# Kernel tuning notes

Hardware: AMD Instinct MI355X
Metric: run time of the kernel (lower is better)

Reference implementation:

```python
import jax, jax.numpy as jnp
import numpy as np

B, T, D, N, R, K = 4, 4096, 1024, 64, 16, 4  # batch, seq, d_model, state_size, dt_rank, conv_kernel


def setup_inputs() -> dict:
    key = jax.random.key(0)
    ks = jax.random.split(key, 6)
    s = 0.02  # small init scale (original uses xavier/zeros; random here for a meaningful baseline)
    return {
        "x": jax.random.normal(ks[0], (B, T, D), jnp.float32),
        "conv_w": jax.random.normal(ks[1], (D, K), jnp.float32) * s,  # depthwise conv kernel [D, K]
        "in_w": jax.random.normal(ks[2], (N, D), jnp.float32) * s,    # input_proj weight
        "in_b": jnp.zeros((N,), jnp.float32),
        "dt_w": jax.random.normal(ks[3], (R, D), jnp.float32) * s,    # delta_proj weight
        "dt_b": jnp.zeros((R,), jnp.float32),
        "tr_w": jax.random.normal(ks[4], (N, R), jnp.float32) * s,    # transition weight (no bias)
        "out_w": jax.random.normal(ks[5], (D, N), jnp.float32) * s,   # output_proj weight
        "out_b": jnp.zeros((D,), jnp.float32),
    }


def reference(x, conv_w, in_w, in_b, dt_w, dt_b, tr_w, out_w, out_b):
    Bx, Tx, Dx = x.shape
    k = conv_w.shape[1]
    # Causal depthwise conv: torch Conv1d(pad=k-1, groups=D) then slice [:T]
    xp = jnp.pad(x, ((0, 0), (k - 1, 0), (0, 0)))  # left-pad time axis
    conv_out = sum(xp[:, j:j + Tx, :] * conv_w[:, j] for j in range(k))  # [B,T,D]
    projected = (x + conv_out) @ in_w.T + in_b                 # [B,T,N]
    delta = jnp.tanh(x @ dt_w.T + dt_b) @ tr_w.T               # [B,T,N]

    def step(state, inp):
        d_t, p_t = inp  # each [B,N]
        state = jax.nn.silu(d_t + state) + p_t
        return state, state

    init = jnp.zeros((Bx, in_w.shape[0]), x.dtype)
    _, states = jax.lax.scan(step, init,
                             (jnp.swapaxes(delta, 0, 1), jnp.swapaxes(projected, 0, 1)))
    states = jnp.swapaxes(states, 0, 1)  # [B,T,N]
    return states @ out_w.T + out_b      # [B,T,D] (dropout=0.0 -> identity)
```

## Files before the change

kernel.cpp:

```cpp
#include <hip/hip_runtime.h>
#include <math.h>

#define Bn 4
#define Tn 4096
#define Dn 1024
#define Nn 64
#define Rn 16
#define KCONV 4

#define TT2 32
#define KCH 32
#define SU 32

typedef __attribute__((ext_vector_type(8))) short bf16x8;
typedef __attribute__((ext_vector_type(4))) float f32x4;

__device__ __forceinline__ unsigned short bf16_rne(float f) {
    unsigned int u = __float_as_uint(f);
    unsigned int r = (u + 0x7fffu + ((u >> 16) & 1u)) >> 16;
    return (unsigned short)r;
}

typedef const __attribute__((address_space(1))) void GVoid;
typedef __attribute__((address_space(3))) void LVoid;
typedef __attribute__((address_space(3))) float LdsFloat;


__global__ __launch_bounds__(256)
void prep0_kernel(const float* __restrict__ in_w, const float* __restrict__ dt_w,
                  unsigned short* __restrict__ ws)
{
    const int kc  = blockIdx.x;
    const int k0  = kc * KCH;
    const int tid = threadIdx.x;
    unsigned short* wsb = ws + (size_t)kc * 5120;

    {
        const int lane = tid & 63;
        const int n = (tid >> 6) * 16 + (lane & 15), s = lane >> 4;
        const float* wp = &in_w[(size_t)n * Dn + k0 + 8 * s];
        float4 a  = *(const float4*)wp;
        float4 bq = *(const float4*)(wp + 4);
        float wv[8] = {a.x, a.y, a.z, a.w, bq.x, bq.y, bq.z, bq.w};
        bf16x8 fh, fl;
        #pragma unroll
        for (int k = 0; k < 8; ++k) {
            unsigned short h = bf16_rne(wv[k]);
            float hf = __uint_as_float((unsigned)h << 16);
            fh[k] = (short)h; fl[k] = (short)bf16_rne(wv[k] - hf);
        }
        *(bf16x8*)&wsb[(size_t)tid * 8]        = fh;
        *(bf16x8*)&wsb[2048 + (size_t)tid * 8] = fl;
    }
    if (tid < 64) {
        const int r = tid & 15, s = tid >> 4;
        const float* wp = &dt_w[(size_t)r * Dn + k0 + 8 * s];
        float4 a  = *(const float4*)wp;
        float4 bq = *(const float4*)(wp + 4);
        float wv[8] = {a.x, a.y, a.z, a.w, bq.x, bq.y, bq.z, bq.w};
        bf16x8 fh, fl;
        #pragma unroll
        for (int k = 0; k < 8; ++k) {
            unsigned short h = bf16_rne(wv[k]);
            float hf = __uint_as_float((unsigned)h << 16);
            fh[k] = (short)h; fl[k] = (short)bf16_rne(wv[k] - hf);
        }
        *(bf16x8*)&wsb[4096 + (size_t)tid * 8] = fh;
        *(bf16x8*)&wsb[4608 + (size_t)tid * 8] = fl;
    }
}

__global__ __launch_bounds__(128)
void prep_kernel(const float* __restrict__ x, const float* __restrict__ conv_w,
                 const unsigned short* __restrict__ ws,
                 const float* __restrict__ in_b, const float* __restrict__ dt_b,
                 const float* __restrict__ tr_w,
                 float* __restrict__ O)
{
    __shared__ bf16x8 Axc_h[2][64], Axc_l[2][64];
    __shared__ bf16x8 Axr_h[2][64], Axr_l[2][64];
    __shared__ bf16x8 Bst[640];
    __shared__ float  xs[35][36];
    __shared__ float4 cws[32];
    __shared__ float  AsS[TT2][17];
    __shared__ float  trS[Nn][17];

    const int tid = threadIdx.x;
    const int b   = blockIdx.y;
    const int t0  = blockIdx.x * TT2;
    const int l   = tid & 63;
    const int w   = tid >> 6;

    const float* xb = x + (size_t)b * Tn * Dn;

    for (int idx = tid; idx < Nn * Rn; idx += 128)
        trS[idx >> 4][idx & 15] = tr_w[idx];

    const f32x4 z4 = {0.f, 0.f, 0.f, 0.f};
    f32x4 accP[4] = {z4, z4, z4, z4};
    f32x4 accG = z4;

    for (int kc = 0; kc < Dn / KCH; ++kc) {
        const int k0 = kc * KCH;
        __syncthreads();

        if (tid < 64) {
            const unsigned short* wsb = ws + (size_t)kc * 5120 + (size_t)l * 8;
            #pragma unroll
            for (int j = 0; j < 10; ++j)
                __builtin_amdgcn_global_load_lds((GVoid*)(wsb + j * 512),
                                                 (LVoid*)(Bst + j * 64), 16, 0, 0);
        }

        {
            const int row  = tid >> 2;
            const int colg = tid & 3;
            const int tp   = t0 - 3 + row;
            float4 a = {0.f,0.f,0.f,0.f}, bq = {0.f,0.f,0.f,0.f};
            if (tp >= 0) {
                const float* src = &xb[(size_t)tp * Dn + k0 + 8 * colg];
                a  = *(const float4*)src;
                bq = *(const float4*)(src + 4);
            }
            *(float4*)&xs[row][8 * colg]     = a;
            *(float4*)&xs[row][8 * colg + 4] = bq;
            if (tid < 12) {
                const int row2 = 32 + (tid >> 2), colg2 = tid & 3;
                const float* s2 = &xb[(size_t)(t0 - 3 + row2) * Dn + k0 + 8 * colg2];
                *(float4*)&xs[row2][8 * colg2]     = *(const float4*)s2;
                *(float4*)&xs[row2][8 * colg2 + 4] = *(const float4*)(s2 + 4);
            }
            if (tid >= 64 && tid < 96)
                cws[tid - 64] = *(const float4*)&conv_w[(size_t)(k0 + tid - 64) * 4];
        }
        __syncthreads();

        {
            const int m = tid & 31;
            const int s = tid >> 5;
            float v[4][8];
            #pragma unroll
            for (int dr = 0; dr < 4; ++dr) {
                float4 a  = *(const float4*)&xs[m + dr][8 * s];
                float4 bq = *(const float4*)&xs[m + dr][8 * s + 4];
                v[dr][0]=a.x;  v[dr][1]=a.y;  v[dr][2]=a.z;  v[dr][3]=a.w;
                v[dr][4]=bq.x; v[dr][5]=bq.y; v[dr][6]=bq.z; v[dr][7]=bq.w;
            }
            bf16x8 fch, fcl, frh, frl;
            #pragma unroll
            for (int k = 0; k < 8; ++k) {
                float4 cw = cws[8 * s + k];
                float xr = v[3][k];
                float xc = xr;
                xc = fmaf(v[0][k], cw.x, xc);
                xc = fmaf(v[1][k], cw.y, xc);
                xc = fmaf(v[2][k], cw.z, xc);
                xc = fmaf(v[3][k], cw.w, xc);
                unsigned short h; float hf;
                h = bf16_rne(xc); hf = __uint_as_float((unsigned)h << 16);
                fch[k] = (short)h; fcl[k] = (short)bf16_rne(xc - hf);
                h = bf16_rne(xr); hf = __uint_as_float((unsigned)h << 16);
                frh[k] = (short)h; frl[k] = (short)bf16_rne(xr - hf);
            }
            const int lane = (m & 15) | (s << 4), mt = m >> 4;
            Axc_h[mt][lane] = fch; Axc_l[mt][lane] = fcl;
            Axr_h[mt][lane] = frh; Axr_l[mt][lane] = frl;
        }
        __syncthreads();

        bf16x8 axh = Axc_h[w][l], axl = Axc_l[w][l];
        bf16x8 arh = Axr_h[w][l], arl = Axr_l[w][l];
        #pragma unroll
        for (int nt = 0; nt < 4; ++nt) {
            bf16x8 bh = Bst[nt * 64 + l];
            bf16x8 bl = Bst[256 + nt * 64 + l];
            accP[nt] = __builtin_amdgcn_mfma_f32_16x16x32_bf16(axh, bh, accP[nt], 0, 0, 0);
            accP[nt] = __builtin_amdgcn_mfma_f32_16x16x32_bf16(axl, bh, accP[nt], 0, 0, 0);
            accP[nt] = __builtin_amdgcn_mfma_f32_16x16x32_bf16(axh, bl, accP[nt], 0, 0, 0);
        }
        {
            bf16x8 bh = Bst[512 + l];
            bf16x8 bl = Bst[576 + l];
            accG = __builtin_amdgcn_mfma_f32_16x16x32_bf16(arh, bh, accG, 0, 0, 0);
            accG = __builtin_amdgcn_mfma_f32_16x16x32_bf16(arl, bh, accG, 0, 0, 0);
            accG = __builtin_amdgcn_mfma_f32_16x16x32_bf16(arh, bl, accG, 0, 0, 0);
        }
    }

    __syncthreads();
    #pragma unroll
    for (int i = 0; i < 4; ++i)
        AsS[16 * w + 4 * (l >> 4) + i][l & 15] = tanhf(accG[i] + dt_b[l & 15]);
    __syncthreads();

    float as_[4][16];
    #pragma unroll
    for (int i = 0; i < 4; ++i) {
        int mrow = 16 * w + 4 * (l >> 4) + i;
        #pragma unroll
        for (int j = 0; j < 4; ++j) {
            float4 q = *(const float4*)&AsS[mrow][4 * j];
            as_[i][4*j] = q.x; as_[i][4*j+1] = q.y;
            as_[i][4*j+2] = q.z; as_[i][4*j+3] = q.w;
        }
    }
    const int tile0 = t0 & ~63;
    const int coff  = t0 & 63;
    #pragma unroll
    for (int nt = 0; nt < 4; ++nt) {
        int n = 16 * nt + (l & 15);
        float tw[16];
        #pragma unroll
        for (int j = 0; j < 4; ++j) {
            float4 q = *(const float4*)&trS[n][4 * j];
            tw[4*j] = q.x; tw[4*j+1] = q.y; tw[4*j+2] = q.z; tw[4*j+3] = q.w;
        }
        float ib = in_b[n];
        #pragma unroll
        for (int i = 0; i < 4; ++i) {
            int mrow = 16 * w + 4 * (l >> 4) + i;
            float dlv = 0.f;
            #pragma unroll
            for (int r = 0; r < 16; ++r) dlv = fmaf(as_[i][r], tw[r], dlv);
            size_t a = ((size_t)(b * Tn + tile0 + n)) * Dn + coff + mrow;
            O[a]      = accP[nt][i] + ib;
            O[a + 64] = dlv;
        }
    }
}


#define WAITV(N) do {                                                    \
    asm volatile("s_waitcnt vmcnt(" #N ")" ::: "memory");                \
    __builtin_amdgcn_sched_barrier(0);                                   \
} while (0)

__device__ __forceinline__ void issue_chunk(float* lds, const float* rp)
{
    #pragma unroll
    for (int j = 0; j < 8; ++j)
        __builtin_amdgcn_global_load_lds((GVoid*)(rp + 4 * j),
                                         (LVoid*)(lds + j * 256), 16, 0, 0);
    #pragma unroll
    for (int j = 0; j < 8; ++j)
        __builtin_amdgcn_global_load_lds((GVoid*)(rp + 64 + 4 * j),
                                         (LVoid*)(lds + (8 + j) * 256), 16, 0, 0);
}

#define DS_READ_ALL(pv, dv, a)                                           \
    asm volatile(                                                        \
        "ds_read_b128 %0, %16 offset:0\n\t"                              \
        "ds_read_b128 %1, %16 offset:1024\n\t"                           \
        "ds_read_b128 %2, %16 offset:2048\n\t"                           \
        "ds_read_b128 %3, %16 offset:3072\n\t"                           \
        "ds_read_b128 %4, %16 offset:4096\n\t"                           \
        "ds_read_b128 %5, %16 offset:5120\n\t"                           \
        "ds_read_b128 %6, %16 offset:6144\n\t"                           \
        "ds_read_b128 %7, %16 offset:7168\n\t"                           \
        "ds_read_b128 %8, %16 offset:8192\n\t"                           \
        "ds_read_b128 %9, %16 offset:9216\n\t"                           \
        "ds_read_b128 %10, %16 offset:10240\n\t"                         \
        "ds_read_b128 %11, %16 offset:11264\n\t"                         \
        "ds_read_b128 %12, %16 offset:12288\n\t"                         \
        "ds_read_b128 %13, %16 offset:13312\n\t"                         \
        "ds_read_b128 %14, %16 offset:14336\n\t"                         \
        "ds_read_b128 %15, %16 offset:15360\n\t"                         \
        "s_waitcnt lgkmcnt(0)"                                           \
        : "=&v"(pv[0]), "=&v"(pv[1]), "=&v"(pv[2]), "=&v"(pv[3]),        \
          "=&v"(pv[4]), "=&v"(pv[5]), "=&v"(pv[6]), "=&v"(pv[7]),        \
          "=&v"(dv[0]), "=&v"(dv[1]), "=&v"(dv[2]), "=&v"(dv[3]),        \
          "=&v"(dv[4]), "=&v"(dv[5]), "=&v"(dv[6]), "=&v"(dv[7])         \
        : "v"(a) : "memory")

__device__ __forceinline__ void scan_chunk(const float* buf, int n, float& st,
                                           f32x4 (&sv)[8], float* sp)
{
    const float L2E = 1.44269504088896340736f;
    if (sp) {
        #pragma unroll
        for (int j = 0; j < 8; ++j)
            *(f32x4*)(sp + 4 * j) = sv[j];
    }
    unsigned a = (unsigned)(unsigned long long)(LdsFloat*)buf
               + (unsigned)(n * 16);
    f32x4 pv[8], dv[8];
    DS_READ_ALL(pv, dv, a);
    __builtin_amdgcn_sched_barrier(0);
    #pragma unroll
    for (int j = 0; j < 8; ++j) {
        #pragma unroll
        for (int i = 0; i < 4; ++i) {
            float d  = dv[j][i];
            float u  = st + d;
            float e  = __builtin_amdgcn_exp2f(fmaf(st, -L2E, -d * L2E));
            float r  = __builtin_amdgcn_rcpf(1.f + e);
            st = fmaf(u, r, pv[j][i]);
            sv[j][i] = st;
        }
    }
}

#define RP(c) (obase + (size_t)((((c) >> 1) * 64) + n) * Dn + ((c) & 1) * 32)
#define SP(c) (RP(c) + 128)

__global__ __launch_bounds__(64, 1)
void scan_kernel(float* __restrict__ O)
{
    __shared__ __align__(16) float buf[3][4096];

    const int b = blockIdx.x;
    const int n = threadIdx.x;
    float* obase = O + (size_t)b * Tn * Dn;

    float* b0 = buf[0];
    float* b1 = buf[1];
    float* b2 = buf[2];

    f32x4 sv[8];
    float st = 0.f;

    issue_chunk(b0, RP(0));
    issue_chunk(b1, RP(1));
    issue_chunk(b2, RP(2));
    WAITV(32);
    scan_chunk(b0, n, st, sv, nullptr);
    { float* t = b0; b0 = b1; b1 = b2; b2 = t; }

    issue_chunk(b2, RP(3));
    WAITV(32);
    scan_chunk(b0, n, st, sv, SP(0));
    { float* t = b0; b0 = b1; b1 = b2; b2 = t; }

    #pragma unroll 1
    for (int c = 2; c <= 125; ++c) {
        issue_chunk(b2, RP(c + 2));
        WAITV(40);
        scan_chunk(b0, n, st, sv, SP(c - 1));
        { float* t = b0; b0 = b1; b1 = b2; b2 = t; }
    }

    WAITV(24);
    scan_chunk(b0, n, st, sv, SP(125));
    { float* t = b0; b0 = b1; b1 = b2; b2 = t; }

    WAITV(16);
    scan_chunk(b0, n, st, sv, SP(126));

    {
        float* sp = SP(127);
        #pragma unroll
        for (int j = 0; j < 8; ++j)
            *(f32x4*)(sp + 4 * j) = sv[j];
    }
}

#undef RP
#undef SP

__global__ __launch_bounds__(256)
void out_kernel(const float* __restrict__ out_w, const float* __restrict__ out_b,
                float* __restrict__ O)
{
    __shared__ float Ss[64][Nn + 4];
    __shared__ float wT[Nn][64 + 4];

    const int tid = threadIdx.x;
    const int r0  = blockIdx.x * 64;
    const int c   = tid & 15;
    const int g   = tid >> 4;

    float4 wreg[4];
    #pragma unroll
    for (int q = 0; q < 4; ++q) {
        int idx = tid + q * 256;
        int dl = idx >> 4, n4 = (idx & 15) * 4;
        wreg[q] = *(const float4*)&out_w[(size_t)dl * Nn + n4];
    }

    for (int idx = tid; idx < 64 * 16; idx += 256) {
        int nn = idx >> 4, tg = idx & 15;
        float4 v = *(const float4*)&O[(size_t)(r0 + nn) * Dn + 128 + 4 * tg];
        Ss[4 * tg + 0][nn] = v.x;
        Ss[4 * tg + 1][nn] = v.y;
        Ss[4 * tg + 2][nn] = v.z;
        Ss[4 * tg + 3][nn] = v.w;
    }
    __syncthreads();

    for (int cb = 0; cb < Dn / 64; ++cb) {
        #pragma unroll
        for (int q = 0; q < 4; ++q) {
            int idx = tid + q * 256;
            int dl = idx >> 4, n4 = (idx & 15) * 4;
            wT[n4 + 0][dl] = wreg[q].x;
            wT[n4 + 1][dl] = wreg[q].y;
            wT[n4 + 2][dl] = wreg[q].z;
            wT[n4 + 3][dl] = wreg[q].w;
        }
        if (cb + 1 < Dn / 64) {
            const int d0n = (cb + 1) * 64;
            #pragma unroll
            for (int q = 0; q < 4; ++q) {
                int idx = tid + q * 256;
                int dl = idx >> 4, n4 = (idx & 15) * 4;
                wreg[q] = *(const float4*)&out_w[(size_t)(d0n + dl) * Nn + n4];
            }
        }
        __syncthreads();

        const int d0 = cb * 64;
        float acc[4][4] = {};
        #pragma unroll
        for (int kq = 0; kq < Nn; kq += 4) {
            float4 wv0 = *(const float4*)&wT[kq + 0][4 * c];
            float4 wv1 = *(const float4*)&wT[kq + 1][4 * c];
            float4 wv2 = *(const float4*)&wT[kq + 2][4 * c];
            float4 wv3 = *(const float4*)&wT[kq + 3][4 * c];
            #pragma unroll
            for (int i = 0; i < 4; ++i) {
                int row = g + 16 * i;
                float4 xv = *(const float4*)&Ss[row][kq];
                acc[i][0] = fmaf(xv.x, wv0.x, fmaf(xv.y, wv1.x, fmaf(xv.z, wv2.x, fmaf(xv.w, wv3.x, acc[i][0]))));
                acc[i][1] = fmaf(xv.x, wv0.y, fmaf(xv.y, wv1.y, fmaf(xv.z, wv2.y, fmaf(xv.w, wv3.y, acc[i][1]))));
                acc[i][2] = fmaf(xv.x, wv0.z, fmaf(xv.y, wv1.z, fmaf(xv.z, wv2.z, fmaf(xv.w, wv3.z, acc[i][2]))));
                acc[i][3] = fmaf(xv.x, wv0.w, fmaf(xv.y, wv1.w, fmaf(xv.z, wv2.w, fmaf(xv.w, wv3.w, acc[i][3]))));
            }
        }

        float4 bb = *(const float4*)&out_b[d0 + 4 * c];
        #pragma unroll
        for (int i = 0; i < 4; ++i) {
            int row = g + 16 * i;
            float4 o = make_float4(acc[i][0] + bb.x, acc[i][1] + bb.y,
                                   acc[i][2] + bb.z, acc[i][3] + bb.w);
            *(float4*)&O[(size_t)(r0 + row) * Dn + d0 + 4 * c] = o;
        }
        __syncthreads();
    }
}

extern "C" void kernel_launch(void* const* d_in, const int* in_sizes, int n_in,
                              void* d_out, int out_size, void* d_ws, size_t ws_size,
                              hipStream_t stream)
{
    const float* x      = (const float*)d_in[0];
    const float* conv_w = (const float*)d_in[1];
    const float* in_w   = (const float*)d_in[2];
    const float* in_b   = (const float*)d_in[3];
    const float* dt_w   = (const float*)d_in[4];
    const float* dt_b   = (const float*)d_in[5];
    const float* tr_w   = (const float*)d_in[6];
    const float* out_w  = (const float*)d_in[7];
    const float* out_b  = (const float*)d_in[8];
    float* O = (float*)d_out;
    unsigned short* ws = (unsigned short*)d_ws;
    (void)ws_size;

    prep0_kernel<<<dim3(Dn / KCH), 256, 0, stream>>>(in_w, dt_w, ws);

    dim3 g1(Tn / TT2, Bn);
    prep_kernel<<<g1, 128, 0, stream>>>(x, conv_w, ws, in_b, dt_b, tr_w, O);

    scan_kernel<<<dim3(Bn), 64, 0, stream>>>(O);

    out_kernel<<<dim3((Bn * Tn) / 64), 256, 0, stream>>>(out_w, out_b, O);
}
```

Before: 337.4 us.

## Move output projection to bf16x3 split MFMA with pre-split weights

The fp32 FMA output projection is replaced by MFMA 16x16x32 bf16 instructions that use a hi/lo split (three products) to keep near-fp32 accuracy. out_w is pre-split into bf16 hi/lo fragments in the prep kernel and streamed into LDS with async global-to-LDS loads, double-buffered per wave. The goal is to cut the out_kernel's ALU-bound time. In exchange the outputs are written as scattered scalar stores, and the bf16x3 scheme carries a small risk of precision loss.

```diff
diff --git a/kernel.cpp b/kernel.cpp
--- a/kernel.cpp
+++ b/kernel.cpp
@@ -28,45 +28,68 @@
 
 __global__ __launch_bounds__(256)
 void prep0_kernel(const float* __restrict__ in_w, const float* __restrict__ dt_w,
-                  unsigned short* __restrict__ ws)
-{
-    const int kc  = blockIdx.x;
-    const int k0  = kc * KCH;
+                  const float* __restrict__ out_w, unsigned short* __restrict__ ws)
+{
     const int tid = threadIdx.x;
-    unsigned short* wsb = ws + (size_t)kc * 5120;
-
-    {
-        const int lane = tid & 63;
-        const int n = (tid >> 6) * 16 + (lane & 15), s = lane >> 4;
-        const float* wp = &in_w[(size_t)n * Dn + k0 + 8 * s];
-        float4 a  = *(const float4*)wp;
-        float4 bq = *(const float4*)(wp + 4);
-        float wv[8] = {a.x, a.y, a.z, a.w, bq.x, bq.y, bq.z, bq.w};
-        bf16x8 fh, fl;
-        #pragma unroll
-        for (int k = 0; k < 8; ++k) {
-            unsigned short h = bf16_rne(wv[k]);
-            float hf = __uint_as_float((unsigned)h << 16);
-            fh[k] = (short)h; fl[k] = (short)bf16_rne(wv[k] - hf);
-        }
-        *(bf16x8*)&wsb[(size_t)tid * 8]        = fh;
-        *(bf16x8*)&wsb[2048 + (size_t)tid * 8] = fl;
-    }
-    if (tid < 64) {
-        const int r = tid & 15, s = tid >> 4;
-        const float* wp = &dt_w[(size_t)r * Dn + k0 + 8 * s];
-        float4 a  = *(const float4*)wp;
-        float4 bq = *(const float4*)(wp + 4);
-        float wv[8] = {a.x, a.y, a.z, a.w, bq.x, bq.y, bq.z, bq.w};
-        bf16x8 fh, fl;
-        #pragma unroll
-        for (int k = 0; k < 8; ++k) {
-            unsigned short h = bf16_rne(wv[k]);
-            float hf = __uint_as_float((unsigned)h << 16);
-            fh[k] = (short)h; fl[k] = (short)bf16_rne(wv[k] - hf);
-        }
-        *(bf16x8*)&wsb[4096 + (size_t)tid * 8] = fh;
-        *(bf16x8*)&wsb[4608 + (size_t)tid * 8] = fl;
+    if (blockIdx.x < 32) {
+        const int kc  = blockIdx.x;
+        const int k0  = kc * KCH;
+        unsigned short* wsb = ws + (size_t)kc * 5120;
+        {
+            const int lane = tid & 63;
+            const int n = (tid >> 6) * 16 + (lane & 15), s = lane >> 4;
+            const float* wp = &in_w[(size_t)n * Dn + k0 + 8 * s];
+            float4 a  = *(const float4*)wp;
+            float4 bq = *(const float4*)(wp + 4);
+            float wv[8] = {a.x, a.y, a.z, a.w, bq.x, bq.y, bq.z, bq.w};
+            bf16x8 fh, fl;
+            #pragma unroll
+            for (int k = 0; k < 8; ++k) {
+                unsigned short h = bf16_rne(wv[k]);
+                float hf = __uint_as_float((unsigned)h << 16);
+                fh[k] = (short)h; fl[k] = (short)bf16_rne(wv[k] - hf);
+            }
+            *(bf16x8*)&wsb[(size_t)tid * 8]        = fh;
+            *(bf16x8*)&wsb[2048 + (size_t)tid * 8] = fl;
+        }
+        if (tid < 64) {
+            const int r = tid & 15, s = tid >> 4;
+            const float* wp = &dt_w[(size_t)r * Dn + k0 + 8 * s];
+            float4 a  = *(const float4*)wp;
+            float4 bq = *(const float4*)(wp + 4);
+            float wv[8] = {a.x, a.y, a.z, a.w, bq.x, bq.y, bq.z, bq.w};
+            bf16x8 fh, fl;
+            #pragma unroll
+            for (int k = 0; k < 8; ++k) {
+                unsigned short h = bf16_rne(wv[k]);
+                float hf = __uint_as_float((unsigned)h << 16);
+                fh[k] = (short)h; fl[k] = (short)bf16_rne(wv[k] - hf);
+            }
+            *(bf16x8*)&wsb[4096 + (size_t)tid * 8] = fh;
+            *(bf16x8*)&wsb[4608 + (size_t)tid * 8] = fl;
+        }
+    } else {
+        const int dt = blockIdx.x - 32;
+        if (tid < 128) {
+            const int kh = tid >> 6, lane = tid & 63;
+            const int d  = dt * 16 + (lane & 15);
+            const int n0 = kh * 32 + (lane >> 4) * 8;
+            const float* wp = &out_w[(size_t)d * Nn + n0];
+            float4 a  = *(const float4*)wp;
+            float4 bq = *(const float4*)(wp + 4);
+            float wv[8] = {a.x, a.y, a.z, a.w, bq.x, bq.y, bq.z, bq.w};
+            bf16x8 fh, fl;
+            #pragma unroll
+            for (int k = 0; k < 8; ++k) {
+                unsigned short h = bf16_rne(wv[k]);
+                float hf = __uint_as_float((unsigned)h << 16);
+                fh[k] = (short)h; fl[k] = (short)bf16_rne(wv[k] - hf);
+            }
+            unsigned short* wsb = ws + 163840 + (size_t)dt * 2048
+                                + (size_t)kh * 1024 + (size_t)lane * 8;
+            *(bf16x8*)wsb         = fh;
+            *(bf16x8*)(wsb + 512) = fl;
+        }
     }
 }
 
@@ -357,25 +380,35 @@
 #undef RP
 #undef SP
 
+
+#define DS_READ_B8(b00h, b00l, b01h, b01l, b10h, b10l, b11h, b11l, a)    \
+    asm volatile(                                                        \
+        "ds_read_b128 %0, %8 offset:0\n\t"                               \
+        "ds_read_b128 %1, %8 offset:1024\n\t"                            \
+        "ds_read_b128 %2, %8 offset:2048\n\t"                            \
+        "ds_read_b128 %3, %8 offset:3072\n\t"                            \
+        "ds_read_b128 %4, %8 offset:4096\n\t"                            \
+        "ds_read_b128 %5, %8 offset:5120\n\t"                            \
+        "ds_read_b128 %6, %8 offset:6144\n\t"                            \
+        "ds_read_b128 %7, %8 offset:7168\n\t"                            \
+        "s_waitcnt lgkmcnt(0)"                                           \
+        : "=&v"(b00h), "=&v"(b00l), "=&v"(b01h), "=&v"(b01l),            \
+          "=&v"(b10h), "=&v"(b10l), "=&v"(b11h), "=&v"(b11l)             \
+        : "v"(a) : "memory")
+
 __global__ __launch_bounds__(256)
-void out_kernel(const float* __restrict__ out_w, const float* __restrict__ out_b,
-                float* __restrict__ O)
-{
-    __shared__ float Ss[64][Nn + 4];
-    __shared__ float wT[Nn][64 + 4];
+void out_kernel(const unsigned short* __restrict__ ws,
+                const float* __restrict__ out_b, float* __restrict__ O)
+{
+    __shared__ float  Ss[64][Nn + 4];
+    __shared__ bf16x8 AfH[8][64], AfL[8][64];
+    __shared__ bf16x8 Bb[4][2][8][64];
 
     const int tid = threadIdx.x;
     const int r0  = blockIdx.x * 64;
-    const int c   = tid & 15;
-    const int g   = tid >> 4;
-
-    float4 wreg[4];
-    #pragma unroll
-    for (int q = 0; q < 4; ++q) {
-        int idx = tid + q * 256;
-        int dl = idx >> 4, n4 = (idx & 15) * 4;
-        wreg[q] = *(const float4*)&out_w[(size_t)dl * Nn + n4];
-    }
+    const int l   = tid & 63;
+    const int w   = tid >> 6;
+    const unsigned short* ws2 = ws + 163840;
 
     for (int idx = tid; idx < 64 * 16; idx += 256) {
         int nn = idx >> 4, tg = idx & 15;
@@ -387,55 +420,90 @@
     }
     __syncthreads();
 
-    for (int cb = 0; cb < Dn / 64; ++cb) {
-        #pragma unroll
-        for (int q = 0; q < 4; ++q) {
-            int idx = tid + q * 256;
-            int dl = idx >> 4, n4 = (idx & 15) * 4;
-            wT[n4 + 0][dl] = wreg[q].x;
-            wT[n4 + 1][dl] = wreg[q].y;
-            wT[n4 + 2][dl] = wreg[q].z;
-            wT[n4 + 3][dl] = wreg[q].w;
-        }
-        if (cb + 1 < Dn / 64) {
-            const int d0n = (cb + 1) * 64;
-            #pragma unroll
-            for (int q = 0; q < 4; ++q) {
-                int idx = tid + q * 256;
-                int dl = idx >> 4, n4 = (idx & 15) * 4;
-                wreg[q] = *(const float4*)&out_w[(size_t)(d0n + dl) * Nn + n4];
-            }
-        }
-        __syncthreads();
-
-        const int d0 = cb * 64;
-        float acc[4][4] = {};
-        #pragma unroll
-        for (int kq = 0; kq < Nn; kq += 4) {
-            float4 wv0 = *(const float4*)&wT[kq + 0][4 * c];
-            float4 wv1 = *(const float4*)&wT[kq + 1][4 * c];
-            float4 wv2 = *(const float4*)&wT[kq + 2][4 * c];
-            float4 wv3 = *(const float4*)&wT[kq + 3][4 * c];
-            #pragma unroll
-            for (int i = 0; i < 4; ++i) {
-                int row = g + 16 * i;
-                float4 xv = *(const float4*)&Ss[row][kq];
-                acc[i][0] = fmaf(xv.x, wv0.x, fmaf(xv.y, wv1.x, fmaf(xv.z, wv2.x, fmaf(xv.w, wv3.x, acc[i][0]))));
-                acc[i][1] = fmaf(xv.x, wv0.y, fmaf(xv.y, wv1.y, fmaf(xv.z, wv2.y, fmaf(xv.w, wv3.y, acc[i][1]))));
-                acc[i][2] = fmaf(xv.x, wv0.z, fmaf(xv.y, wv1.z, fmaf(xv.z, wv2.z, fmaf(xv.w, wv3.z, acc[i][2]))));
-                acc[i][3] = fmaf(xv.x, wv0.w, fmaf(xv.y, wv1.w, fmaf(xv.z, wv2.w, fmaf(xv.w, wv3.w, acc[i][3]))));
-            }
-        }
-
-        float4 bb = *(const float4*)&out_b[d0 + 4 * c];
-        #pragma unroll
-        for (int i = 0; i < 4; ++i) {
-            int row = g + 16 * i;
-            float4 o = make_float4(acc[i][0] + bb.x, acc[i][1] + bb.y,
-                                   acc[i][2] + bb.z, acc[i][3] + bb.w);
-            *(float4*)&O[(size_t)(r0 + row) * Dn + d0 + 4 * c] = o;
-        }
-        __syncthreads();
+    #pragma unroll
+    for (int s2 = 0; s2 < 2; ++s2) {
+        int slot = tid + s2 * 256;
+        int grp = slot >> 6, ln = slot & 63;
+        int tt = grp & 3, kh = grp >> 2;
+        int t  = tt * 16 + (ln & 15);
+        int n0 = kh * 32 + (ln >> 4) * 8;
+        float4 q0 = *(const float4*)&Ss[t][n0];
+        float4 q1 = *(const float4*)&Ss[t][n0 + 4];
+        float v[8] = {q0.x, q0.y, q0.z, q0.w, q1.x, q1.y, q1.z, q1.w};
+        bf16x8 fh, fl;
+        #pragma unroll
+        for (int k = 0; k < 8; ++k) {
+            unsigned short h = bf16_rne(v[k]);
+            float hf = __uint_as_float((unsigned)h << 16);
+            fh[k] = (short)h; fl[k] = (short)bf16_rne(v[k] - hf);
+        }
+        AfH[grp][ln] = fh; AfL[grp][ln] = fl;
+    }
+    __syncthreads();
+
+    bf16x8 ah[4][2], al[4][2];
+    #pragma unroll
+    for (int tt = 0; tt < 4; ++tt)
+        #pragma unroll
+        for (int kh = 0; kh < 2; ++kh) {
+            ah[tt][kh] = AfH[kh * 4 + tt][l];
+            al[tt][kh] = AfL[kh * 4 + tt][l];
+        }
+    float ob[16];
+    #pragma unroll
+    for (int k = 0; k < 16; ++k)
+        ob[k] = out_b[(w * 16 + k) * 16 + (l & 15)];
+
+    const unsigned bbase = (unsigned)(unsigned long long)(LdsFloat*)&Bb[w][0][0][0]
+                         + (unsigned)(l * 16);
+    const f32x4 z4 = {0.f, 0.f, 0.f, 0.f};
+
+    {
+        const unsigned short* p = ws2 + (size_t)(w * 16) * 2048 + l * 8;
+        #pragma unroll
+        for (int g = 0; g < 8; ++g)
+            __builtin_amdgcn_global_load_lds((GVoid*)(p + (g >> 2) * 2048 + (g & 3) * 512),
+                                             (LVoid*)&Bb[w][0][g][0], 16, 0, 0);
+    }
+
+    #pragma unroll
+    for (int i = 0; i < 8; ++i) {
+        if (i < 7) {
+            const unsigned short* p = ws2 + (size_t)(w * 16 + 2 * (i + 1)) * 2048 + l * 8;
+            #pragma unroll
+            for (int g = 0; g < 8; ++g)
+                __builtin_amdgcn_global_load_lds((GVoid*)(p + (g >> 2) * 2048 + (g & 3) * 512),
+                                                 (LVoid*)&Bb[w][(i + 1) & 1][g][0], 16, 0, 0);
+            WAITV(8);
+        } else {
+            WAITV(0);
+        }
+        unsigned a = bbase + (unsigned)((i & 1) * 8192);
+        bf16x8 bh[2][2], bl[2][2];
+        DS_READ_B8(bh[0][0], bl[0][0], bh[0][1], bl[0][1],
+                   bh[1][0], bl[1][0], bh[1][1], bl[1][1], a);
+        __builtin_amdgcn_sched_barrier(0);
+
+        #pragma unroll
+        for (int dto = 0; dto < 2; ++dto) {
+            const int dcol = (w * 16 + 2 * i + dto) * 16 + (l & 15);
+            const float bbv = ob[2 * i + dto];
+            #pragma unroll
+            for (int tt = 0; tt < 4; ++tt) {
+                f32x4 acc = z4;
+                #pragma unroll
+                for (int kh = 0; kh < 2; ++kh) {
+                    acc = __builtin_amdgcn_mfma_f32_16x16x32_bf16(ah[tt][kh], bh[dto][kh], acc, 0, 0, 0);
+                    acc = __builtin_amdgcn_mfma_f32_16x16x32_bf16(al[tt][kh], bh[dto][kh], acc, 0, 0, 0);
+                    acc = __builtin_amdgcn_mfma_f32_16x16x32_bf16(ah[tt][kh], bl[dto][kh], acc, 0, 0, 0);
+                }
+                #pragma unroll
+                for (int j = 0; j < 4; ++j) {
+                    int row = tt * 16 + (l >> 4) * 4 + j;
+                    O[(size_t)(r0 + row) * Dn + dcol] = acc[j] + bbv;
+                }
+            }
+        }
     }
 }
 
@@ -456,12 +524,12 @@
     unsigned short* ws = (unsigned short*)d_ws;
     (void)ws_size;
 
-    prep0_kernel<<<dim3(Dn / KCH), 256, 0, stream>>>(in_w, dt_w, ws);
+    prep0_kernel<<<dim3(96), 256, 0, stream>>>(in_w, dt_w, out_w, ws);
 
     dim3 g1(Tn / TT2, Bn);
     prep_kernel<<<g1, 128, 0, stream>>>(x, conv_w, ws, in_b, dt_b, tr_w, O);
 
     scan_kernel<<<dim3(Bn), 64, 0, stream>>>(O);
 
-    out_kernel<<<dim3((Bn * Tn) / 64), 256, 0, stream>>>(out_w, out_b, O);
-}
+    out_kernel<<<dim3((Bn * Tn) / 64), 256, 0, stream>>>(ws, out_b, O);
+}
```

New measurement: 306.7 us. 1.1x faster.
